# Performance work log

Hardware: AMD Instinct MI355X
Metric: run time of the kernel (lower is better)

The kernel has to match this reference:

```python
import jax, jax.numpy as jnp
import numpy as np

N = 50000      # nodes
E = 800000     # edges (avg degree 16)
IN = 128       # in_channels
C = 64         # hidden_channels (per-head out channels)
H = 8          # heads


def _lin(key, fan_in, fan_out):
    kw, kb = jax.random.split(key)
    scale = 1.0 / np.sqrt(fan_in)
    W = jax.random.uniform(kw, (fan_in, fan_out), jnp.float32, -scale, scale)
    b = jax.random.uniform(kb, (fan_out,), jnp.float32, -scale, scale)
    return W, b


def setup_inputs() -> dict:
    key = jax.random.key(0)
    ks = jax.random.split(key, 16)
    inp = {
        'x': jax.random.normal(ks[0], (N, IN), jnp.float32),
        'edge_index': jax.random.randint(ks[1], (2, E), 0, N, jnp.int64),
    }
    # layer 0: IN -> H*C (concat), layer 1: H*C -> H*C (concat), layer 2: H*C -> C (heads=1)
    dims = [(IN, H * C, H * C), (H * C, H * C, H * C), (H * C, C, C)]
    k = 2
    for i, (fi, fqkv, fskip) in enumerate(dims):
        for nm, fo in (('Wq', fqkv), ('Wk', fqkv), ('Wv', fqkv), ('Ws', fskip)):
            W, b = _lin(ks[k], fi, fo)
            inp[f'{nm}{i}'] = W
            inp[f'b{nm[1]}{i}'] = b
            k += 1
    return inp


def _conv(x, src, dst, Wq, bq, Wk, bk, Wv, bv, Ws, bs, heads, ch, concat):
    n = x.shape[0]
    q = (x @ Wq + bq).reshape(n, heads, ch)   # [N,H,C]
    k = (x @ Wk + bk).reshape(n, heads, ch)
    v = (x @ Wv + bv).reshape(n, heads, ch)
    # per-edge attention logits: [E,H]
    alpha = jnp.einsum('ehc,ehc->eh', q[dst], k[src]) / (ch ** 0.5)
    # segment softmax over incoming edges of each target node
    m = jax.ops.segment_max(alpha, dst, num_segments=n)
    m = jnp.where(jnp.isfinite(m), m, 0.0)
    ea = jnp.exp(alpha - m[dst])
    denom = jax.ops.segment_sum(ea, dst, num_segments=n) + 1e-16
    attn = ea / denom[dst]                    # [E,H]
    out = jax.ops.segment_sum(attn[:, :, None] * v[src], dst, num_segments=n)  # [N,H,C]
    out = out.reshape(n, heads * ch) if concat else out.mean(axis=1)
    # root/skip connection (beta=False)
    return out + x @ Ws + bs


def reference(x, edge_index,
              Wq0, bq0, Wk0, bk0, Wv0, bv0, Ws0, bs0,
              Wq1, bq1, Wk1, bk1, Wv1, bv1, Ws1, bs1,
              Wq2, bq2, Wk2, bk2, Wv2, bv2, Ws2, bs2):
    src, dst = edge_index[0], edge_index[1]
    h = _conv(x, src, dst, Wq0, bq0, Wk0, bk0, Wv0, bv0, Ws0, bs0, H, C, True)
    h = jax.nn.relu(h)
    h = _conv(h, src, dst, Wq1, bq1, Wk1, bk1, Wv1, bv1, Ws1, bs1, H, C, True)
    h = jax.nn.relu(h)
    out = _conv(h, src, dst, Wq2, bq2, Wk2, bk2, Wv2, bv2, Ws2, bs2, 1, C, False)
    return out
```

## Files before the change

kernel.cpp:

```cpp
#include <hip/hip_runtime.h>
#include <hip/hip_fp16.h>
#include <math.h>
#include <stdio.h>


using f16x8 = __attribute__((ext_vector_type(8))) _Float16;
using f32x4 = __attribute__((ext_vector_type(4))) float;

__device__ __forceinline__ void load_lds16(const void* g, void* l) {
  __builtin_amdgcn_global_load_lds((const __attribute__((address_space(1))) void*)g,
                                   (__attribute__((address_space(3))) void*)l,
                                   16, 0, 0);
}

__device__ __forceinline__ void fp8x4_to_f32(unsigned int w, float* o4) {
#if __has_builtin(__builtin_amdgcn_cvt_pk_f32_fp8)
  auto lo = __builtin_amdgcn_cvt_pk_f32_fp8(w, false);
  auto hi = __builtin_amdgcn_cvt_pk_f32_fp8(w, true);
  o4[0] = lo[0]; o4[1] = lo[1]; o4[2] = hi[0]; o4[3] = hi[1];
#else
#pragma unroll
  for (int t = 0; t < 4; ++t) {
    unsigned int b = (w >> (8 * t)) & 0xFFu;
    unsigned short h = (unsigned short)(((b & 0x80u) << 8) | ((b & 0x7Fu) << 7));
    __half hv = *(__half*)&h;
    o4[t] = (float)hv * 256.0f;
  }
#endif
}

__device__ __forceinline__ unsigned int fp8_pack2(float a, float b) {
#if __has_builtin(__builtin_amdgcn_cvt_pk_fp8_f32)
  return (unsigned int)__builtin_amdgcn_cvt_pk_fp8_f32(a, b, 0, false) & 0xFFFFu;
#else
  unsigned int r = 0;
#pragma unroll
  for (int t = 0; t < 2; ++t) {
    float f = t ? b : a;
    __half h = __float2half(f * (1.0f / 256.0f));
    unsigned short hb = *(unsigned short*)&h;
    unsigned int sign = (hb >> 8) & 0x80u;
    unsigned int mag = (hb & 0x7FFFu) + 0x40u;
    unsigned int e = (mag >> 7) & 0x7Fu;
    if ((mag >> 7) > 0x7Eu) e = 0x7Eu;
    r |= (sign | e) << (8 * t);
  }
  return r;
#endif
}

__global__ void zero_misc_kernel(int* __restrict__ deg, __half* __restrict__ H,
                                 int N, int Npad) {
  int t = blockIdx.x * 256 + threadIdx.x;
  if (t < N) deg[t] = 0;
  int nz = (Npad - N) * 512 / 8;
  if (t < nz) {
    f16x8 z = {};
    *(f16x8*)(H + (size_t)N * 512 + (size_t)t * 8) = z;
  }
}

__global__ void degree_kernel(const int* __restrict__ dst, int* __restrict__ deg, int E) {
  int e = blockIdx.x * blockDim.x + threadIdx.x;
  if (e < E) atomicAdd(&deg[dst[e]], 1);
}

__global__ __launch_bounds__(256)
void scan_a_kernel(const int* __restrict__ deg, int* __restrict__ rowptr,
                   int* __restrict__ bsum, int n) {
  __shared__ int tmp[256];
  int t = threadIdx.x;
  int i = blockIdx.x * 256 + t;
  int v = (i < n) ? deg[i] : 0;
  tmp[t] = v;
  __syncthreads();
#pragma unroll
  for (int off = 1; off < 256; off <<= 1) {
    int u = (t >= off) ? tmp[t - off] : 0;
    __syncthreads();
    tmp[t] += u;
    __syncthreads();
  }
  if (i < n) rowptr[i + 1] = tmp[t];
  if (t == 255) bsum[blockIdx.x] = tmp[255];
}

__global__ __launch_bounds__(256)
void scan_b_kernel(int* __restrict__ bsum, int nb) {
  __shared__ int tmp[256];
  int t = threadIdx.x;
  int v = (t < nb) ? bsum[t] : 0;
  tmp[t] = v;
  __syncthreads();
#pragma unroll
  for (int off = 1; off < 256; off <<= 1) {
    int u = (t >= off) ? tmp[t - off] : 0;
    __syncthreads();
    tmp[t] += u;
    __syncthreads();
  }
  if (t < nb) bsum[t] = tmp[t] - v;
}

__global__ __launch_bounds__(256)
void scan_c_kernel(int* __restrict__ rowptr, int* __restrict__ cursor,
                   const int* __restrict__ bsum, int n) {
  int i = blockIdx.x * 256 + threadIdx.x;
  if (i < n) {
    int r = rowptr[i + 1] + bsum[blockIdx.x];
    rowptr[i + 1] = r;
    cursor[i + 1] = r;
  }
  if (i == 0) { rowptr[0] = 0; cursor[0] = 0; }
}

__global__ void scatter_kernel(const int* __restrict__ src, const int* __restrict__ dst,
                               int* __restrict__ cursor, int* __restrict__ col, int E) {
  int e = blockIdx.x * blockDim.x + threadIdx.x;
  if (e < E) {
    int pos = atomicAdd(&cursor[dst[e]], 1);
    col[pos] = src[e];
  }
}

__global__ __launch_bounds__(256)
void transpose_all_kernel(
    const float* __restrict__ Wq0, const float* __restrict__ Wk0,
    const float* __restrict__ Wv0, const float* __restrict__ Ws0,
    const float* __restrict__ Wq1, const float* __restrict__ Wk1,
    const float* __restrict__ Wv1, const float* __restrict__ Ws1,
    const float* __restrict__ Wq2, const float* __restrict__ Wk2,
    const float* __restrict__ Wv2, const float* __restrict__ Ws2,
    __half* __restrict__ Wt) {
  int z = blockIdx.z;
  int layer = z >> 2, m = z & 3;
  int K = (layer == 0) ? 128 : 512;
  int D = (layer == 2) ? 64 : 512;
  int c0 = blockIdx.x * 32, k0 = blockIdx.y * 32;
  if (c0 >= D || k0 >= K) return;
  const float* W;
  switch (z) {
    case 0: W = Wq0; break; case 1: W = Wk0; break;
    case 2: W = Wv0; break; case 3: W = Ws0; break;
    case 4: W = Wq1; break; case 5: W = Wk1; break;
    case 6: W = Wv1; break; case 7: W = Ws1; break;
    case 8: W = Wq2; break; case 9: W = Wk2; break;
    case 10: W = Wv2; break; default: W = Ws2; break;
  }
  __half* dstBase = Wt + ((layer == 0) ? 0 : (layer == 1) ? 262144 : 1310720);
  __shared__ float t[32][33];
  int tx = threadIdx.x & 31, ty = threadIdx.x >> 5;
#pragma unroll
  for (int r = 0; r < 4; ++r)
    t[ty + 8 * r][tx] = W[(size_t)(k0 + ty + 8 * r) * D + c0 + tx];
  __syncthreads();
#pragma unroll
  for (int r = 0; r < 4; ++r)
    dstBase[(size_t)(m * D + c0 + ty + 8 * r) * K + k0 + tx] =
        __float2half(t[tx][ty + 8 * r]);
}

__global__ void bias_all_kernel(
    const float* __restrict__ b0, const float* __restrict__ b1,
    const float* __restrict__ b2, const float* __restrict__ b3,
    const float* __restrict__ b4, const float* __restrict__ b5,
    const float* __restrict__ b6, const float* __restrict__ b7,
    const float* __restrict__ b8, const float* __restrict__ b9,
    const float* __restrict__ b10, const float* __restrict__ b11,
    float* __restrict__ bias_arena) {
  int z = blockIdx.x;
  int layer = z >> 2, m = z & 3;
  int D = (layer == 2) ? 64 : 512;
  const float* b;
  switch (z) {
    case 0: b = b0; break; case 1: b = b1; break;
    case 2: b = b2; break; case 3: b = b3; break;
    case 4: b = b4; break; case 5: b = b5; break;
    case 6: b = b6; break; case 7: b = b7; break;
    case 8: b = b8; break; case 9: b = b9; break;
    case 10: b = b10; break; default: b = b11; break;
  }
  float* dst = bias_arena + ((layer == 0) ? 0 : (layer == 1) ? 2048 : 4096) + m * D;
  for (int c = threadIdx.x; c < D; c += 256) dst[c] = b[c];
}

template <int LAYER>
__global__ __launch_bounds__(256, 2)
void gemm_mfma_kernel(const void* __restrict__ Avoid,
                      const __half* __restrict__ Wt,
                      const float* __restrict__ bias,
                      __half* __restrict__ QS, __half* __restrict__ KV,
                      int Nrows) {
  constexpr int K = (LAYER == 0) ? 128 : 512;
  constexpr int lda = (LAYER == 0) ? 128 : 512;
  constexpr int NT = (LAYER == 2) ? 1 : 8;
  __shared__ __align__(16) __half As[128 * 64];
  __shared__ __align__(16) __half Bs[256 * 64];
  int tid = threadIdx.x;
  int wave = tid >> 6, lane = tid & 63;
  int wr = wave >> 1, wc = wave & 1;
  int bid = blockIdx.x;
  int xcd = bid & 7;
  int r = bid >> 3;
  int n0 = (r % NT) * 256;
  int m0 = ((r / NT) * 8 + xcd) * 128;
  int srow = lane >> 3;
  int sslot = lane & 7;
  int skc = (sslot ^ srow) << 3;
  int quad = lane >> 4, rr = lane & 15;

  f32x4 acc[4][8] = {};

  for (int kt = 0; kt < K; kt += 64) {
#pragma unroll
    for (int p = 0; p < 4; ++p) {
      int rbase = wave * 32 + p * 8;
      if constexpr (LAYER == 0) {
        int row = m0 + rbase + srow;
        const float* ga = (const float*)Avoid + (size_t)row * lda + kt + skc;
        f16x8 hv = {};
        if (row < Nrows) {
          float4 f0 = *(const float4*)ga;
          float4 f1 = *(const float4*)(ga + 4);
          hv[0] = (_Float16)f0.x; hv[1] = (_Float16)f0.y;
          hv[2] = (_Float16)f0.z; hv[3] = (_Float16)f0.w;
          hv[4] = (_Float16)f1.x; hv[5] = (_Float16)f1.y;
          hv[6] = (_Float16)f1.z; hv[7] = (_Float16)f1.w;
        }
        *(f16x8*)&As[(rbase + srow) * 64 + sslot * 8] = hv;
      } else {
        const __half* ga = (const __half*)Avoid +
                           (size_t)(m0 + rbase + srow) * lda + kt + skc;
        load_lds16(ga, &As[rbase * 64]);
      }
    }
#pragma unroll
    for (int p = 0; p < 8; ++p) {
      int rbase = wave * 64 + p * 8;
      const __half* gb = Wt + (size_t)(n0 + rbase + srow) * K + kt + skc;
      load_lds16(gb, &Bs[rbase * 64]);
    }
    __syncthreads();
#pragma unroll
    for (int h = 0; h < 2; ++h) {
      int c = h * 4 + quad;
      f16x8 a[4], b[8];
#pragma unroll
      for (int i = 0; i < 4; ++i) {
        int row = wr * 64 + i * 16 + rr;
        a[i] = *(const f16x8*)&As[row * 64 + ((c ^ (row & 7)) << 3)];
      }
#pragma unroll
      for (int j = 0; j < 8; ++j) {
        int row = wc * 128 + j * 16 + rr;
        b[j] = *(const f16x8*)&Bs[row * 64 + ((c ^ (row & 7)) << 3)];
      }
#pragma unroll
      for (int i = 0; i < 4; ++i)
#pragma unroll
        for (int j = 0; j < 8; ++j)
          acc[i][j] = __builtin_amdgcn_mfma_f32_16x16x32_f16(a[i], b[j], acc[i][j], 0, 0, 0);
    }
    __syncthreads();
  }

  int cl = lane & 15, rb = (lane >> 4) * 4;
  if constexpr (LAYER == 2) {
    constexpr int D = 64;
    constexpr int rstride = 128;
#pragma unroll
    for (int j = 0; j < 8; ++j) {
      int gc = n0 + wc * 128 + j * 16 + cl;
      float bj = bias[gc];
      int mseg = gc >> 6;
      int off = gc & (D - 1);
      bool toKV = (mseg == 1) || (mseg == 2);
      __half* base = toKV ? (KV + off + (mseg == 2 ? D : 0))
                          : (QS + off + (mseg == 3 ? D : 0));
#pragma unroll
      for (int i = 0; i < 4; ++i) {
#pragma unroll
        for (int rg = 0; rg < 4; ++rg) {
          int gr = m0 + wr * 64 + i * 16 + rb + rg;
          base[(size_t)gr * rstride] = __float2half(acc[i][j][rg] + bj);
        }
      }
    }
  } else {
    unsigned char* KV8 = (unsigned char*)KV;
#pragma unroll
    for (int j = 0; j < 8; ++j) {
      int gc = n0 + wc * 128 + j * 16 + cl;
      float bj = bias[gc];
      int mseg = gc >> 9;
      int c = gc & 511;
      if (mseg == 0 || mseg == 3) {
        __half* base = QS + c + (mseg == 3 ? 512 : 0);
#pragma unroll
        for (int i = 0; i < 4; ++i) {
#pragma unroll
          for (int rg = 0; rg < 4; ++rg) {
            int gr = m0 + wr * 64 + i * 16 + rb + rg;
            base[(size_t)gr * 1024] = __float2half(acc[i][j][rg] + bj);
          }
        }
      } else {
        unsigned char* base = KV8 + ((c >> 3) * 16 + (c & 7) + (mseg == 2 ? 8 : 0));
#pragma unroll
        for (int i = 0; i < 4; ++i) {
          int gr = m0 + wr * 64 + i * 16 + rb;
          unsigned int w01 = fp8_pack2(acc[i][j][0] + bj, acc[i][j][1] + bj);
          unsigned int w23 = fp8_pack2(acc[i][j][2] + bj, acc[i][j][3] + bj);
          base[(size_t)gr * 1024] = (unsigned char)w01;
          base[(size_t)(gr + 1) * 1024] = (unsigned char)(w01 >> 8);
          base[(size_t)(gr + 2) * 1024] = (unsigned char)w23;
          base[(size_t)(gr + 3) * 1024] = (unsigned char)(w23 >> 8);
        }
      }
    }
  }
}

__global__ __launch_bounds__(256)
void attn_h8_kernel(const __half* __restrict__ QS, const unsigned char* __restrict__ KV8,
                    const int* __restrict__ rowptr, const int* __restrict__ col,
                    __half* __restrict__ Hout, int N) {
  int n = blockIdx.x * 4 + (threadIdx.x >> 6);
  if (n >= N) return;
  int lane = threadIdx.x & 63;
  size_t rbase = (size_t)n * 1024 + lane * 8;

  f16x8 qv = __builtin_nontemporal_load((const f16x8*)(QS + rbase));
  float qf[8];
#pragma unroll
  for (int j = 0; j < 8; ++j) qf[j] = (float)qv[j];

  int e0 = rowptr[n], e1 = rowptr[n + 1];
  float m = -INFINITY, l = 0.f;
  float o[8] = {};

  const uint4* KVL = (const uint4*)KV8;
  uint4 ea = {}, eb = {};
  int i = e0;
  if (i < e1)     ea = KVL[(size_t)col[i] * 64 + lane];
  if (i + 1 < e1) eb = KVL[(size_t)col[i + 1] * 64 + lane];

  while (i < e1) {
    int rem = e1 - i;
    uint4 ec = {}, ed = {};
    if (rem > 2) ec = KVL[(size_t)col[i + 2] * 64 + lane];
    if (rem > 3) ed = KVL[(size_t)col[i + 3] * 64 + lane];
    float ka[8], kb[8];
    fp8x4_to_f32(ea.x, ka); fp8x4_to_f32(ea.y, ka + 4);
    fp8x4_to_f32(eb.x, kb); fp8x4_to_f32(eb.y, kb + 4);
    float pa = 0.f, pb = 0.f;
#pragma unroll
    for (int j = 0; j < 8; ++j) { pa += ka[j] * qf[j]; pb += kb[j] * qf[j]; }
    pa += __shfl_xor(pa, 1, 64); pb += __shfl_xor(pb, 1, 64);
    pa += __shfl_xor(pa, 2, 64); pb += __shfl_xor(pb, 2, 64);
    pa += __shfl_xor(pa, 4, 64); pb += __shfl_xor(pb, 4, 64);
    float a0 = pa * 0.125f;
    float va[8];
    fp8x4_to_f32(ea.z, va); fp8x4_to_f32(ea.w, va + 4);
    if (rem > 1) {
      float vb[8];
      fp8x4_to_f32(eb.z, vb); fp8x4_to_f32(eb.w, vb + 4);
      float a1 = pb * 0.125f;
      float mn = fmaxf(m, fmaxf(a0, a1));
      float sc = __expf(m - mn);
      float ex0 = __expf(a0 - mn), ex1 = __expf(a1 - mn);
      l = l * sc + ex0 + ex1;
#pragma unroll
      for (int c = 0; c < 8; ++c)
        o[c] = o[c] * sc + ex0 * va[c] + ex1 * vb[c];
      m = mn;
    } else {
      float mn = fmaxf(m, a0);
      float sc = __expf(m - mn);
      float ex0 = __expf(a0 - mn);
      l = l * sc + ex0;
#pragma unroll
      for (int c = 0; c < 8; ++c) o[c] = o[c] * sc + ex0 * va[c];
      m = mn;
    }
    ea = ec; eb = ed;
    i += 2;
  }

  float inv = 1.f / (l + 1e-16f);
  f16x8 sv = __builtin_nontemporal_load((const f16x8*)(QS + rbase + 512));
  f16x8 hv;
#pragma unroll
  for (int c = 0; c < 8; ++c) {
    float r = o[c] * inv + (float)sv[c];
    hv[c] = (_Float16)fmaxf(r, 0.f);
  }
  __builtin_nontemporal_store(hv, (f16x8*)(Hout + (size_t)n * 512 + lane * 8));
}

__global__ __launch_bounds__(256)
void attn_h1_kernel(const __half* __restrict__ QS, const __half* __restrict__ KV,
                    const int* __restrict__ rowptr, const int* __restrict__ col,
                    float* __restrict__ out, int N) {
  int n = (blockIdx.x * 256 + threadIdx.x) >> 3;
  if (n >= N) return;
  int gl = threadIdx.x & 7;
  size_t rbase = (size_t)n * 128 + gl * 8;

  f16x8 qv = __builtin_nontemporal_load((const f16x8*)(QS + rbase));
  float qf[8];
#pragma unroll
  for (int j = 0; j < 8; ++j) qf[j] = (float)qv[j];

  int e0 = rowptr[n], e1 = rowptr[n + 1];
  float m = -INFINITY, l = 0.f;
  float o[8] = {};

  f16x8 ka = {}, va = {}, kb = {}, vb = {};
  int i = e0;
  if (i < e1) {
    const __half* p = KV + (size_t)col[i] * 128 + gl * 8;
    ka = *(const f16x8*)p; va = *(const f16x8*)(p + 64);
  }
  if (i + 1 < e1) {
    const __half* p = KV + (size_t)col[i + 1] * 128 + gl * 8;
    kb = *(const f16x8*)p; vb = *(const f16x8*)(p + 64);
  }

  while (i < e1) {
    int rem = e1 - i;
    f16x8 kc = {}, vc = {}, kd = {}, vd = {};
    if (rem > 2) {
      const __half* p = KV + (size_t)col[i + 2] * 128 + gl * 8;
      kc = *(const f16x8*)p; vc = *(const f16x8*)(p + 64);
    }
    if (rem > 3) {
      const __half* p = KV + (size_t)col[i + 3] * 128 + gl * 8;
      kd = *(const f16x8*)p; vd = *(const f16x8*)(p + 64);
    }
    float pa = 0.f, pb = 0.f;
#pragma unroll
    for (int j = 0; j < 8; ++j) { pa += (float)ka[j] * qf[j]; pb += (float)kb[j] * qf[j]; }
    pa += __shfl_xor(pa, 1, 64); pb += __shfl_xor(pb, 1, 64);
    pa += __shfl_xor(pa, 2, 64); pb += __shfl_xor(pb, 2, 64);
    pa += __shfl_xor(pa, 4, 64); pb += __shfl_xor(pb, 4, 64);
    float a0 = pa * 0.125f;
    if (rem > 1) {
      float a1 = pb * 0.125f;
      float mn = fmaxf(m, fmaxf(a0, a1));
      float sc = __expf(m - mn);
      float ea = __expf(a0 - mn), eb = __expf(a1 - mn);
      l = l * sc + ea + eb;
#pragma unroll
      for (int c = 0; c < 8; ++c)
        o[c] = o[c] * sc + ea * (float)va[c] + eb * (float)vb[c];
      m = mn;
    } else {
      float mn = fmaxf(m, a0);
      float sc = __expf(m - mn);
      float ea = __expf(a0 - mn);
      l = l * sc + ea;
#pragma unroll
      for (int c = 0; c < 8; ++c) o[c] = o[c] * sc + ea * (float)va[c];
      m = mn;
    }
    ka = kc; va = vc; kb = kd; vb = vd;
    i += 2;
  }

  float inv = 1.f / (l + 1e-16f);
  f16x8 sv = __builtin_nontemporal_load((const f16x8*)(QS + rbase + 64));
  f32x4 r0, r1;
#pragma unroll
  for (int c = 0; c < 4; ++c) r0[c] = o[c] * inv + (float)sv[c];
#pragma unroll
  for (int c = 0; c < 4; ++c) r1[c] = o[c + 4] * inv + (float)sv[c + 4];
  float* op = out + (size_t)n * 64 + gl * 8;
  *(f32x4*)op = r0;
  *(f32x4*)(op + 4) = r1;
}

extern "C" void kernel_launch(void* const* d_in, const int* in_sizes, int n_in,
                              void* d_out, int out_size, void* d_ws, size_t ws_size,
                              hipStream_t stream) {
  const float* x = (const float*)d_in[0];
  const int* ei = (const int*)d_in[1];
  const int N = in_sizes[0] / 128;
  const int E = in_sizes[1] / 2;
  const int Npad = ((N + 1023) / 1024) * 1024;
  const int mtiles = Npad / 128;
  const int* srcp = ei;
  const int* dstp = ei + E;

  const float* Wq0 = (const float*)d_in[2];  const float* bq0 = (const float*)d_in[3];
  const float* Wk0 = (const float*)d_in[4];  const float* bk0 = (const float*)d_in[5];
  const float* Wv0 = (const float*)d_in[6];  const float* bv0 = (const float*)d_in[7];
  const float* Ws0 = (const float*)d_in[8];  const float* bs0 = (const float*)d_in[9];
  const float* Wq1 = (const float*)d_in[10]; const float* bq1 = (const float*)d_in[11];
  const float* Wk1 = (const float*)d_in[12]; const float* bk1 = (const float*)d_in[13];
  const float* Wv1 = (const float*)d_in[14]; const float* bv1 = (const float*)d_in[15];
  const float* Ws1 = (const float*)d_in[16]; const float* bs1 = (const float*)d_in[17];
  const float* Wq2 = (const float*)d_in[18]; const float* bq2 = (const float*)d_in[19];
  const float* Wk2 = (const float*)d_in[20]; const float* bk2 = (const float*)d_in[21];
  const float* Wv2 = (const float*)d_in[22]; const float* bv2 = (const float*)d_in[23];
  const float* Ws2 = (const float*)d_in[24]; const float* bs2 = (const float*)d_in[25];

  char* p = (char*)d_ws;
  __half* QS = (__half*)p;               p += (size_t)Npad * 1024 * 2;
  __half* KV = (__half*)p;               p += (size_t)Npad * 1024;
  __half* H  = (__half*)p;               p += (size_t)Npad * 512 * 2;
  __half* Wt = (__half*)p;               p += (size_t)1441792 * 2;
  float* bias_arena = (float*)p;         p += 4352 * 4;
  int* deg    = (int*)p;                 p += (size_t)N * 4;
  int* rowptr = (int*)p;                 p += (size_t)(N + 1) * 4;
  int* cursor = (int*)p;                 p += (size_t)(N + 1) * 4;
  int* colv   = (int*)p;                 p += (size_t)E * 4;
  int* bsum   = (int*)p;                 p += 256 * 4;
  size_t need = p - (char*)d_ws;
  if (ws_size < need) {
    fprintf(stderr, "kernel_launch: ws_size=%zu < need=%zu — aborting cleanly\n",
            ws_size, need);
    return;
  }

  const int nscan = (N + 255) / 256;

  transpose_all_kernel<<<dim3(16, 16, 12), 256, 0, stream>>>(
      Wq0, Wk0, Wv0, Ws0, Wq1, Wk1, Wv1, Ws1, Wq2, Wk2, Wv2, Ws2, Wt);
  bias_all_kernel<<<12, 256, 0, stream>>>(
      bq0, bk0, bv0, bs0, bq1, bk1, bv1, bs1, bq2, bk2, bv2, bs2, bias_arena);
  zero_misc_kernel<<<((Npad - N) * 512 / 8 + 255) / 256 > (N + 255) / 256
                         ? ((Npad - N) * 512 / 8 + 255) / 256
                         : (N + 255) / 256,
                    256, 0, stream>>>(deg, H, N, Npad);

  degree_kernel<<<(E + 255) / 256, 256, 0, stream>>>(dstp, deg, E);
  scan_a_kernel<<<nscan, 256, 0, stream>>>(deg, rowptr, bsum, N);
  scan_b_kernel<<<1, 256, 0, stream>>>(bsum, nscan);
  scan_c_kernel<<<nscan, 256, 0, stream>>>(rowptr, cursor, bsum, N);
  scatter_kernel<<<(E + 255) / 256, 256, 0, stream>>>(srcp, dstp, cursor, colv, E);

  __half* Wt0 = Wt;
  __half* Wt1 = Wt + 262144;
  __half* Wt2 = Wt + 1310720;

  gemm_mfma_kernel<0><<<mtiles * 8, 256, 0, stream>>>(
      x, Wt0, bias_arena, QS, KV, N);
  attn_h8_kernel<<<(N + 3) / 4, 256, 0, stream>>>(QS, (const unsigned char*)KV,
                                                  rowptr, colv, H, N);

  gemm_mfma_kernel<1><<<mtiles * 8, 256, 0, stream>>>(
      H, Wt1, bias_arena + 2048, QS, KV, Npad);
  attn_h8_kernel<<<(N + 3) / 4, 256, 0, stream>>>(QS, (const unsigned char*)KV,
                                                  rowptr, colv, H, N);

  gemm_mfma_kernel<2><<<mtiles, 256, 0, stream>>>(
      H, Wt2, bias_arena + 4096, QS, KV, Npad);
  attn_h1_kernel<<<(N + 31) / 32, 256, 0, stream>>>(QS, KV, rowptr, colv,
                                                    (float*)d_out, N);
}
```

Before: 752.5 us.

## Stage GEMM epilogue through LDS for coalesced vector stores

The GEMM epilogue used to write each output element as a scattered 2-byte half or 1-byte fp8 store along columns. It now stages accumulator tiles, with bias added, in LDS (reusing the A/B shared buffer) and writes back 16-byte f16x8 or 8-byte packed-fp8 vectors that are coalesced along rows. fp8 packing now converts eight values at a time with the hardware packed-convert builtin. Launch bounds are raised to 3 blocks per CU, which adds register pressure and several extra barriers in exchange for far fewer memory transactions.

```diff
diff --git a/kernel.cpp b/kernel.cpp
--- a/kernel.cpp
+++ b/kernel.cpp
@@ -29,10 +29,7 @@
 #endif
 }
 
-__device__ __forceinline__ unsigned int fp8_pack2(float a, float b) {
-#if __has_builtin(__builtin_amdgcn_cvt_pk_fp8_f32)
-  return (unsigned int)__builtin_amdgcn_cvt_pk_fp8_f32(a, b, 0, false) & 0xFFFFu;
-#else
+__device__ __forceinline__ unsigned int fp8_pack2_sw(float a, float b) {
   unsigned int r = 0;
 #pragma unroll
   for (int t = 0; t < 2; ++t) {
@@ -45,6 +42,20 @@
     if ((mag >> 7) > 0x7Eu) e = 0x7Eu;
     r |= (sign | e) << (8 * t);
   }
+  return r;
+}
+
+__device__ __forceinline__ uint2 fp8_pack8(const float* f) {
+#if __has_builtin(__builtin_amdgcn_cvt_pk_fp8_f32)
+  int w0 = __builtin_amdgcn_cvt_pk_fp8_f32(f[0], f[1], 0, false);
+  w0 = __builtin_amdgcn_cvt_pk_fp8_f32(f[2], f[3], w0, true);
+  int w1 = __builtin_amdgcn_cvt_pk_fp8_f32(f[4], f[5], 0, false);
+  w1 = __builtin_amdgcn_cvt_pk_fp8_f32(f[6], f[7], w1, true);
+  uint2 r; r.x = (unsigned)w0; r.y = (unsigned)w1; return r;
+#else
+  uint2 r;
+  r.x = fp8_pack2_sw(f[0], f[1]) | (fp8_pack2_sw(f[2], f[3]) << 16);
+  r.y = fp8_pack2_sw(f[4], f[5]) | (fp8_pack2_sw(f[6], f[7]) << 16);
   return r;
 #endif
 }
@@ -185,7 +196,7 @@
 }
 
 template <int LAYER>
-__global__ __launch_bounds__(256, 2)
+__global__ __launch_bounds__(256, 3)
 void gemm_mfma_kernel(const void* __restrict__ Avoid,
                       const __half* __restrict__ Wt,
                       const float* __restrict__ bias,
@@ -194,8 +205,9 @@
   constexpr int K = (LAYER == 0) ? 128 : 512;
   constexpr int lda = (LAYER == 0) ? 128 : 512;
   constexpr int NT = (LAYER == 2) ? 1 : 8;
-  __shared__ __align__(16) __half As[128 * 64];
-  __shared__ __align__(16) __half Bs[256 * 64];
+  __shared__ __align__(16) char smem_raw[49152];
+  __half* As = (__half*)smem_raw;
+  __half* Bs = (__half*)smem_raw + 8192;
   int tid = threadIdx.x;
   int wave = tid >> 6, lane = tid & 63;
   int wr = wave >> 1, wc = wave & 1;
@@ -265,57 +277,113 @@
   }
 
   int cl = lane & 15, rb = (lane >> 4) * 4;
+
   if constexpr (LAYER == 2) {
-    constexpr int D = 64;
-    constexpr int rstride = 128;
-#pragma unroll
-    for (int j = 0; j < 8; ++j) {
-      int gc = n0 + wc * 128 + j * 16 + cl;
-      float bj = bias[gc];
-      int mseg = gc >> 6;
-      int off = gc & (D - 1);
-      bool toKV = (mseg == 1) || (mseg == 2);
-      __half* base = toKV ? (KV + off + (mseg == 2 ? D : 0))
-                          : (QS + off + (mseg == 3 ? D : 0));
-#pragma unroll
-      for (int i = 0; i < 4; ++i) {
-#pragma unroll
-        for (int rg = 0; rg < 4; ++rg) {
-          int gr = m0 + wr * 64 + i * 16 + rb + rg;
-          base[(size_t)gr * rstride] = __float2half(acc[i][j][rg] + bj);
+    __half* S = (__half*)smem_raw;
+#pragma unroll
+    for (int round = 0; round < 2; ++round) {
+      if (wr == round) {
+#pragma unroll
+        for (int i = 0; i < 4; ++i)
+#pragma unroll
+          for (int j = 0; j < 8; ++j) {
+            int colL = wc * 128 + j * 16 + cl;
+            float bj = bias[colL];
+#pragma unroll
+            for (int rg = 0; rg < 4; ++rg) {
+              int rowL = i * 16 + rb + rg;
+              S[rowL * 264 + colL] = __float2half(acc[i][j][rg] + bj);
+            }
+          }
+      }
+      __syncthreads();
+#pragma unroll
+      for (int it = 0; it < 8; ++it) {
+        int id = it * 256 + tid;
+        int rowL = id >> 5, ch = id & 31;
+        int grow = m0 + round * 64 + rowL;
+        int colb = ch * 8;
+        int seg = colb >> 6, c = colb & 63;
+        __half* base = (seg == 0) ? QS + (size_t)grow * 128 + c
+                     : (seg == 3) ? QS + (size_t)grow * 128 + 64 + c
+                     : (seg == 1) ? KV + (size_t)grow * 128 + c
+                                  : KV + (size_t)grow * 128 + 64 + c;
+        *(f16x8*)base = *(const f16x8*)&S[rowL * 264 + colb];
+      }
+      __syncthreads();
+    }
+  } else {
+    const int msegB = n0 >> 9;
+    const int cb = n0 & 511;
+    if (msegB == 0 || msegB == 3) {
+      __half* S = (__half*)smem_raw;
+      const int coff = (msegB == 3) ? 512 : 0;
+#pragma unroll
+      for (int round = 0; round < 2; ++round) {
+        if (wr == round) {
+#pragma unroll
+          for (int i = 0; i < 4; ++i)
+#pragma unroll
+            for (int j = 0; j < 8; ++j) {
+              int colL = wc * 128 + j * 16 + cl;
+              float bj = bias[n0 + colL];
+#pragma unroll
+              for (int rg = 0; rg < 4; ++rg) {
+                int rowL = i * 16 + rb + rg;
+                S[rowL * 264 + colL] = __float2half(acc[i][j][rg] + bj);
+              }
+            }
         }
+        __syncthreads();
+#pragma unroll
+        for (int it = 0; it < 8; ++it) {
+          int id = it * 256 + tid;
+          int rowL = id >> 5, ch = id & 31;
+          int grow = m0 + round * 64 + rowL;
+          int colb = ch * 8;
+          *(f16x8*)(QS + (size_t)grow * 1024 + coff + cb + colb) =
+              *(const f16x8*)&S[rowL * 264 + colb];
+        }
+        __syncthreads();
       }
-    }
-  } else {
-    unsigned char* KV8 = (unsigned char*)KV;
-#pragma unroll
-    for (int j = 0; j < 8; ++j) {
-      int gc = n0 + wc * 128 + j * 16 + cl;
-      float bj = bias[gc];
-      int mseg = gc >> 9;
-      int c = gc & 511;
-      if (mseg == 0 || mseg == 3) {
-        __half* base = QS + c + (mseg == 3 ? 512 : 0);
-#pragma unroll
-        for (int i = 0; i < 4; ++i) {
-#pragma unroll
-          for (int rg = 0; rg < 4; ++rg) {
-            int gr = m0 + wr * 64 + i * 16 + rb + rg;
-            base[(size_t)gr * 1024] = __float2half(acc[i][j][rg] + bj);
+    } else {
+      float* S = (float*)smem_raw;
+      unsigned char* KV8 = (unsigned char*)KV;
+      const int koff = (msegB == 2) ? 8 : 0;
+#pragma unroll
+      for (int round = 0; round < 4; ++round) {
+        if (wr == (round >> 1)) {
+          constexpr int dummy = 0; (void)dummy;
+#pragma unroll
+          for (int ii = 0; ii < 2; ++ii) {
+#pragma unroll
+            for (int j = 0; j < 8; ++j) {
+              int colL = wc * 128 + j * 16 + cl;
+              float bj = bias[n0 + colL];
+#pragma unroll
+              for (int rg = 0; rg < 4; ++rg) {
+                int rowL = ii * 16 + rb + rg;
+                S[rowL * 260 + colL] = acc[(round & 1) * 2 + ii][j][rg] + bj;
+              }
+            }
           }
         }
-      } else {
-        unsigned char* base = KV8 + ((c >> 3) * 16 + (c & 7) + (mseg == 2 ? 8 : 0));
-#pragma unroll
-        for (int i = 0; i < 4; ++i) {
-          int gr = m0 + wr * 64 + i * 16 + rb;
-          unsigned int w01 = fp8_pack2(acc[i][j][0] + bj, acc[i][j][1] + bj);
-          unsigned int w23 = fp8_pack2(acc[i][j][2] + bj, acc[i][j][3] + bj);
-          base[(size_t)gr * 1024] = (unsigned char)w01;
-          base[(size_t)(gr + 1) * 1024] = (unsigned char)(w01 >> 8);
-          base[(size_t)(gr + 2) * 1024] = (unsigned char)w23;
-          base[(size_t)(gr + 3) * 1024] = (unsigned char)(w23 >> 8);
+        __syncthreads();
+#pragma unroll
+        for (int it = 0; it < 4; ++it) {
+          int id = it * 256 + tid;
+          int rowL = id >> 5, ch = id & 31;
+          int grow = m0 + round * 32 + rowL;
+          int colb = ch * 8;
+          float f[8];
+          f32x4 lo = *(const f32x4*)&S[rowL * 260 + colb];
+          f32x4 hi = *(const f32x4*)&S[rowL * 260 + colb + 4];
+          f[0] = lo[0]; f[1] = lo[1]; f[2] = lo[2]; f[3] = lo[3];
+          f[4] = hi[0]; f[5] = hi[1]; f[6] = hi[2]; f[7] = hi[3];
+          uint2 pk = fp8_pack8(f);
+          *(uint2*)(KV8 + (size_t)grow * 1024 + ((cb + colb) >> 3) * 16 + koff) = pk;
         }
+        __syncthreads();
       }
     }
   }
```

Result: slower. 1.313 ms (+74.4%).
